# Kernel optimization log

Measured on AMD Instinct MI355X. Metric: run time of the kernel, lower is better.

Reference implementation:

```python
import jax, jax.numpy as jnp
import numpy as np

V, B, N, D, L, H = 30522, 32, 512, 512, 4, 8
HD = D // H
REC = L // 2  # block-recurrent layer index
SCALE = HD ** -0.5


def _ln(x, g, b):
    m = x.mean(-1, keepdims=True)
    v = ((x - m) ** 2).mean(-1, keepdims=True)
    return (x - m) / jnp.sqrt(v + 1e-5) * g + b


def _rope(t):
    # t: [b,h,n,hd]; rotary embedding on token positions (split-half convention)
    n = t.shape[2]
    inv = 1.0 / (10000.0 ** (jnp.arange(0, HD, 2, dtype=jnp.float32) / HD))
    f = jnp.arange(n, dtype=jnp.float32)[:, None] * inv  # [n, hd/2]
    cos, sin = jnp.cos(f), jnp.sin(f)
    t1, t2 = t[..., : HD // 2], t[..., HD // 2 :]
    return jnp.concatenate([t1 * cos - t2 * sin, t2 * cos + t1 * sin], -1)


def _heads(x):
    b, n, _ = x.shape
    return x.reshape(b, n, H, HD).transpose(0, 2, 1, 3)


def _merge(x):
    b, h, n, d = x.shape
    return x.transpose(0, 2, 1, 3).reshape(b, n, h * d)


def _attn(q, k, v, mask):
    s = jnp.einsum('bhid,bhjd->bhij', q, k) * SCALE
    if mask is not None:
        s = jnp.where(mask, s, jnp.float32(-1e9))
    a = jax.nn.softmax(s, axis=-1)
    return jnp.einsum('bhij,bhjd->bhid', a, v)


def setup_inputs() -> dict:
    key = jax.random.key(0)
    ks = jax.random.split(key, 12)
    w = lambda k, shp: jax.random.normal(k, shp, jnp.float32) * 0.02
    return {
        'ids': jax.random.randint(ks[0], (B, N), 0, V),
        'state': jax.random.normal(ks[1], (B, D), jnp.float32),
        'tok_emb': w(ks[2], (V, D)),
        'ln1_g': jnp.ones((L, D), jnp.float32), 'ln1_b': jnp.zeros((L, D), jnp.float32),
        'w_qkv': w(ks[3], (L, D, 3 * D)),
        'w_o': w(ks[4], (L, D, D)),
        'ln2_g': jnp.ones((L, D), jnp.float32), 'ln2_b': jnp.zeros((L, D), jnp.float32),
        'w_ff1': w(ks[5], (L, D, 4 * D)), 'b_ff1': jnp.zeros((L, 4 * D), jnp.float32),
        'w_ff2': w(ks[6], (L, 4 * D, D)), 'b_ff2': jnp.zeros((L, D), jnp.float32),
        's_ln_g': jnp.ones((D,), jnp.float32), 's_ln_b': jnp.zeros((D,), jnp.float32),
        'w_s_qkv': w(ks[7], (D, 3 * D)),
        'w_so': w(ks[8], (D, D)),
        'gate_beta': w(ks[9], (D,)),
        'f_ln_g': jnp.ones((D,), jnp.float32), 'f_ln_b': jnp.zeros((D,), jnp.float32),
        'head_w': w(ks[10], (D, 1)), 'head_b': jnp.zeros((1,), jnp.float32),
    }


def reference(ids, state, tok_emb, ln1_g, ln1_b, w_qkv, w_o, ln2_g, ln2_b,
              w_ff1, b_ff1, w_ff2, b_ff2, s_ln_g, s_ln_b, w_s_qkv, w_so,
              gate_beta, f_ln_g, f_ln_b, head_w, head_b):
    x = tok_emb[ids]                       # [b,n,d]
    s = state[:, None, :]                  # [b,1,d]  (state.unsqueeze(1))
    n = x.shape[1]
    causal = jnp.tril(jnp.ones((n, n), bool))
    for l in range(L):
        h = _ln(x, ln1_g[l], ln1_b[l])
        q, k, v = jnp.split(h @ w_qkv[l], 3, axis=-1)
        q, k, v = _heads(q), _heads(k), _heads(v)
        q, k = _rope(q), _rope(k)
        if l == REC:
            sn = _ln(s, s_ln_g, s_ln_b)
            sq, sk, sv = jnp.split(sn @ w_s_qkv, 3, axis=-1)
            sq, sk, sv = _heads(sq), _heads(sk), _heads(sv)
            # tokens attend over [tokens (causal), state vector (always visible)]
            m = jnp.concatenate([causal, jnp.ones((n, 1), bool)], axis=1)
            out_x = _attn(q, jnp.concatenate([k, sk], 2), jnp.concatenate([v, sv], 2), m)
            x = x + _merge(out_x) @ w_o[l]
            # state attends over [state, all tokens] (no mask)
            out_s = _attn(sq, jnp.concatenate([sk, k], 2), jnp.concatenate([sv, v], 2), None)
            upd = _merge(out_s) @ w_so
            g = jax.nn.sigmoid(gate_beta)   # fixed learned-EMA gate
            s = s * g + upd * (1.0 - g)
        else:
            out_x = _attn(q, k, v, causal)
            x = x + _merge(out_x) @ w_o[l]
        h2 = _ln(x, ln2_g[l], ln2_b[l])
        x = x + jax.nn.gelu(h2 @ w_ff1[l] + b_ff1[l]) @ w_ff2[l] + b_ff2[l]
    x = _ln(x, f_ln_g, f_ln_b)
    state_out = s[:, 0, :]                 # state[0].squeeze()
    logits = x @ head_w + head_b           # [b,n,1]
    out = jax.nn.log_softmax(logits, axis=-1)
    return out, state_out
```

## Files before the change

### kernel.cpp

```cpp
#include <hip/hip_runtime.h>
#include <hip/hip_bf16.h>
#include <math.h>

#define B_ 32
#define N_ 512
#define D_ 512
#define H_ 8
#define HD_ 64
#define QKV_ 1536
#define SCALE_ 0.125f

typedef unsigned short u16;
typedef unsigned int u32;
typedef __attribute__((ext_vector_type(8))) short bf16x8;
typedef __attribute__((ext_vector_type(4))) float f32x4;

#define GLOBAL_AS __attribute__((address_space(1)))
#define LDS_AS __attribute__((address_space(3)))

__device__ __forceinline__ float gelu_f(float x) {
  float u = 0.7978845608028654f * (x + 0.044715f * x * x * x);
  u = fminf(fmaxf(u, -15.f), 15.f);
  float e = __expf(2.f * u);
  float th = 1.f - 2.f * __builtin_amdgcn_rcpf(e + 1.f);
  return 0.5f * x * (1.0f + th);
}

__device__ __forceinline__ u16 f2b(float f) {
  union { float f; u32 u; } v;
  v.f = f;
  u32 r = (v.u + 0x7FFFu + ((v.u >> 16) & 1u)) >> 16;
  return (u16)r;
}

__device__ __forceinline__ float b2f(u16 x) {
  union { u32 u; float f; } v;
  v.u = ((u32)x) << 16;
  return v.f;
}

__device__ __forceinline__ int xcd_swz(int orig, int nwg) {
  int q = nwg >> 3, r = nwg & 7;
  int xcd = orig & 7, idx = orig >> 3;
  return (xcd < r ? xcd * (q + 1) : r * (q + 1) + (xcd - r) * q) + idx;
}

__global__ void k_zero(float* __restrict__ p) {
  p[blockIdx.x * 256 + threadIdx.x] = 0.0f;
}

__global__ void k_rtab(float2* __restrict__ tab) {
  int idx = blockIdx.x * 256 + threadIdx.x;
  int n = idx >> 5, i = idx & 31;
  float inv = powf(10000.0f, -(float)i * (1.0f / 32.0f));
  float f = (float)n * inv;
  float s, c;
  sincosf(f, &s, &c);
  tab[idx] = make_float2(c, s);
}

__global__ void k_embed(const int* __restrict__ ids, const float* __restrict__ emb,
                        float* __restrict__ x) {
  int row = blockIdx.x;
  int id = ids[row];
  const float4* s = (const float4*)(emb + (size_t)id * D_);
  float4* d = (float4*)(x + (size_t)row * D_);
  d[threadIdx.x] = s[threadIdx.x];
}

__global__ void k_wt(const float* __restrict__ W, u16* __restrict__ Wt, int K, int N) {
  __shared__ float tile[32][33];
  int k0 = blockIdx.y * 32, n0 = blockIdx.x * 32;
  int t = threadIdx.x;
  int r = t >> 3, c4 = (t & 7) * 4;
  float4 v = *(const float4*)&W[(size_t)(k0 + r) * N + n0 + c4];
  tile[r][c4] = v.x; tile[r][c4 + 1] = v.y; tile[r][c4 + 2] = v.z; tile[r][c4 + 3] = v.w;
  __syncthreads();
  ushort4 o;
  o.x = f2b(tile[c4 + 0][r]); o.y = f2b(tile[c4 + 1][r]);
  o.z = f2b(tile[c4 + 2][r]); o.w = f2b(tile[c4 + 3][r]);
  *(ushort4*)&Wt[(size_t)(n0 + r) * K + k0 + c4] = o;
}

template <int BF16OUT>
__global__ void k_ln(const float* __restrict__ in, const float* __restrict__ gw,
                     const float* __restrict__ bw, void* __restrict__ outv) {
  int row = blockIdx.x;
  int lane = threadIdx.x;
  const float* p = in + (size_t)row * D_ + lane * 8;
  float4 v0 = *(const float4*)p;
  float4 v1 = *(const float4*)(p + 4);
  float s = v0.x + v0.y + v0.z + v0.w + v1.x + v1.y + v1.z + v1.w;
  float q = v0.x * v0.x + v0.y * v0.y + v0.z * v0.z + v0.w * v0.w +
            v1.x * v1.x + v1.y * v1.y + v1.z * v1.z + v1.w * v1.w;
#pragma unroll
  for (int o = 32; o >= 1; o >>= 1) {
    s += __shfl_xor(s, o);
    q += __shfl_xor(q, o);
  }
  float mean = s * (1.0f / D_);
  float var = q * (1.0f / D_) - mean * mean;
  float rstd = rsqrtf(var + 1e-5f);
  float4 g0 = *(const float4*)(gw + lane * 8);
  float4 g1 = *(const float4*)(gw + lane * 8 + 4);
  float4 b0 = *(const float4*)(bw + lane * 8);
  float4 b1 = *(const float4*)(bw + lane * 8 + 4);
  float o8[8];
  o8[0] = (v0.x - mean) * rstd * g0.x + b0.x;
  o8[1] = (v0.y - mean) * rstd * g0.y + b0.y;
  o8[2] = (v0.z - mean) * rstd * g0.z + b0.z;
  o8[3] = (v0.w - mean) * rstd * g0.w + b0.w;
  o8[4] = (v1.x - mean) * rstd * g1.x + b1.x;
  o8[5] = (v1.y - mean) * rstd * g1.y + b1.y;
  o8[6] = (v1.z - mean) * rstd * g1.z + b1.z;
  o8[7] = (v1.w - mean) * rstd * g1.w + b1.w;
  if (BF16OUT) {
    u16* op = (u16*)outv + (size_t)row * D_ + lane * 8;
    ushort4 a, b;
    a.x = f2b(o8[0]); a.y = f2b(o8[1]); a.z = f2b(o8[2]); a.w = f2b(o8[3]);
    b.x = f2b(o8[4]); b.y = f2b(o8[5]); b.z = f2b(o8[6]); b.w = f2b(o8[7]);
    *(ushort4*)op = a;
    *(ushort4*)(op + 4) = b;
  } else {
    float* op = (float*)outv + (size_t)row * D_ + lane * 8;
    *(float4*)op = make_float4(o8[0], o8[1], o8[2], o8[3]);
    *(float4*)(op + 4) = make_float4(o8[4], o8[5], o8[6], o8[7]);
  }
}

template <int EPI, int BF16OUT>
__global__ __launch_bounds__(256) void k_mgemm(
    const u16* __restrict__ A, const u16* __restrict__ Bt,
    const float* __restrict__ bias, const float* __restrict__ resid,
    void* __restrict__ Cv, int M, int K, int Nc, int nb0) {
  __shared__ u16 As[128 * 32];
  __shared__ u16 Bs[128 * 32];
  int t = threadIdx.x;
  int wave = t >> 6, lane = t & 63;
  int nwg = gridDim.x * gridDim.y;
  int swz = xcd_swz(blockIdx.y * gridDim.x + blockIdx.x, nwg);
  int m0 = (swz / gridDim.x) * 128;
  int n0 = ((swz % gridDim.x) + nb0) * 128;
  int wr = wave >> 1, wc = wave & 1;
  f32x4 acc[4][4] = {};

  int srow = lane >> 2;
  int scol = (lane & 3) * 8;

  for (int k0 = 0; k0 < K; k0 += 32) {
#pragma unroll
    for (int i = 0; i < 2; ++i) {
      int rbase = wave * 32 + i * 16;
      const u16* ga = A + (size_t)(m0 + rbase + srow) * K + k0 + scol;
      __builtin_amdgcn_global_load_lds((const GLOBAL_AS void*)ga,
                                       (LDS_AS void*)&As[rbase * 32], 16, 0, 0);
      const u16* gb = Bt + (size_t)(n0 + rbase + srow) * K + k0 + scol;
      __builtin_amdgcn_global_load_lds((const GLOBAL_AS void*)gb,
                                       (LDS_AS void*)&Bs[rbase * 32], 16, 0, 0);
    }
    __syncthreads();
    bf16x8 af[4], bfr[4];
#pragma unroll
    for (int mi = 0; mi < 4; ++mi)
      af[mi] = *(const bf16x8*)&As[(wr * 64 + mi * 16 + (lane & 15)) * 32 + (lane >> 4) * 8];
#pragma unroll
    for (int ni = 0; ni < 4; ++ni)
      bfr[ni] = *(const bf16x8*)&Bs[(wc * 64 + ni * 16 + (lane & 15)) * 32 + (lane >> 4) * 8];
#pragma unroll
    for (int mi = 0; mi < 4; ++mi)
#pragma unroll
      for (int ni = 0; ni < 4; ++ni)
        acc[mi][ni] = __builtin_amdgcn_mfma_f32_16x16x32_bf16(bfr[ni], af[mi], acc[mi][ni], 0, 0, 0);
    __syncthreads();
  }

#pragma unroll
  for (int mi = 0; mi < 4; ++mi) {
    int m = m0 + wr * 64 + mi * 16 + (lane & 15);
    size_t rowoff = (size_t)m * Nc;
#pragma unroll
    for (int ni = 0; ni < 4; ++ni) {
      int n = n0 + wc * 64 + ni * 16 + (lane >> 4) * 4;
      float v0 = acc[mi][ni][0], v1 = acc[mi][ni][1],
            v2 = acc[mi][ni][2], v3 = acc[mi][ni][3];
      if (EPI == 2 || EPI == 3) {
        float4 bb = *(const float4*)&bias[n];
        v0 += bb.x; v1 += bb.y; v2 += bb.z; v3 += bb.w;
      }
      if (EPI == 2) {
        v0 = gelu_f(v0); v1 = gelu_f(v1); v2 = gelu_f(v2); v3 = gelu_f(v3);
      }
      if (EPI == 1 || EPI == 3) {
        float4 rr = *(const float4*)&resid[rowoff + n];
        v0 += rr.x; v1 += rr.y; v2 += rr.z; v3 += rr.w;
      }
      if (BF16OUT) {
        ushort4 o;
        o.x = f2b(v0); o.y = f2b(v1); o.z = f2b(v2); o.w = f2b(v3);
        *(ushort4*)&((u16*)Cv)[rowoff + n] = o;
      } else {
        *(float4*)&((float*)Cv)[rowoff + n] = make_float4(v0, v1, v2, v3);
      }
    }
  }
}

template <int EPI>
__global__ __launch_bounds__(256) void k_gemm(const float* __restrict__ A,
                                              const float* __restrict__ W,
                                              const float* __restrict__ bias,
                                              const float* __restrict__ resid,
                                              float* __restrict__ C,
                                              int M, int K, int Nc) {
  __shared__ float As[32][68];
  __shared__ float Bs[32][68];
  int t = threadIdx.x;
  int tx = t & 15, ty = t >> 4;
  int m0 = blockIdx.y * 64, n0 = blockIdx.x * 64;
  float acc[4][4] = {};
  int ar = t >> 2, akc = (t & 3) * 8;
  int bkr = t >> 3, bnc = (t & 7) * 8;
  int garow = m0 + ar;
  bool aval = garow < M;
  const float* Aptr = A + (size_t)(aval ? garow : 0) * K + akc;
  const float* Wptr = W + (size_t)bkr * Nc + n0 + bnc;

  for (int k0 = 0; k0 < K; k0 += 32) {
    float4 a0, a1;
    if (aval) {
      a0 = *(const float4*)(Aptr + k0);
      a1 = *(const float4*)(Aptr + k0 + 4);
    } else {
      a0 = make_float4(0.f, 0.f, 0.f, 0.f);
      a1 = a0;
    }
    As[akc + 0][ar] = a0.x; As[akc + 1][ar] = a0.y;
    As[akc + 2][ar] = a0.z; As[akc + 3][ar] = a0.w;
    As[akc + 4][ar] = a1.x; As[akc + 5][ar] = a1.y;
    As[akc + 6][ar] = a1.z; As[akc + 7][ar] = a1.w;
    float4 b0 = *(const float4*)(Wptr + (size_t)k0 * Nc);
    float4 b1 = *(const float4*)(Wptr + (size_t)k0 * Nc + 4);
    *(float4*)&Bs[bkr][bnc] = b0;
    *(float4*)&Bs[bkr][bnc + 4] = b1;
    __syncthreads();
#pragma unroll
    for (int k = 0; k < 32; ++k) {
      float4 av = *(float4*)&As[k][ty * 4];
      float4 bv = *(float4*)&Bs[k][tx * 4];
      float a[4] = {av.x, av.y, av.z, av.w};
      float b[4] = {bv.x, bv.y, bv.z, bv.w};
#pragma unroll
      for (int i = 0; i < 4; ++i)
#pragma unroll
        for (int j = 0; j < 4; ++j) acc[i][j] += a[i] * b[j];
    }
    __syncthreads();
  }
#pragma unroll
  for (int i = 0; i < 4; ++i) {
    int m = m0 + ty * 4 + i;
    if (m >= M) break;
    size_t off = (size_t)m * Nc + n0 + tx * 4;
    float r[4];
#pragma unroll
    for (int j = 0; j < 4; ++j) {
      float v = acc[i][j];
      if (EPI == 2 || EPI == 3) v += bias[n0 + tx * 4 + j];
      if (EPI == 2) v = gelu_f(v);
      if (EPI == 1 || EPI == 3) v += resid[off + j];
      r[j] = v;
    }
    *(float4*)&C[off] = make_float4(r[0], r[1], r[2], r[3]);
  }
}

__global__ __launch_bounds__(512) void k_fattn(const u16* __restrict__ qkv,
                                               const float2* __restrict__ tab,
                                               u16* __restrict__ out) {
  __shared__ u16 Kl[64 * 64];
  __shared__ u16 Vt[64 * 64];
  __shared__ u16 Pl[8][16 * 64];
  int swz = xcd_swz(blockIdx.x, gridDim.x);
  int qt = swz & 3, h = (swz >> 2) & 7, b = swz >> 5;
  int t = threadIdx.x;
  int w = t >> 6, lane = t & 63;
  int c = lane & 15, g = lane >> 4;

  bf16x8 qa[2];
  {
    int n = qt * 128 + w * 16 + c;
    const u16* qptr = qkv + (size_t)(b * N_ + n) * QKV_ + h * HD_ + g * 8;
    union { bf16x8 v; u16 s[8]; } a0, a1, r0, r1;
    a0.v = *(const bf16x8*)qptr;
    a1.v = *(const bf16x8*)(qptr + 32);
    const float2* tb = tab + n * 32 + g * 8;
#pragma unroll
    for (int j = 0; j < 8; ++j) {
      float2 cs = tb[j];
      float lo = b2f(a0.s[j]), hi = b2f(a1.s[j]);
      r0.s[j] = f2b(lo * cs.x - hi * cs.y);
      r1.s[j] = f2b(hi * cs.x + lo * cs.y);
    }
    qa[0] = r0.v;
    qa[1] = r1.v;
  }

  f32x4 O[4] = {};
  float m_r[4], l_r[4];
#pragma unroll
  for (int r = 0; r < 4; ++r) { m_r[r] = -1e30f; l_r[r] = 0.f; }

  int myblk = 2 * qt + (w >> 2);
  int ktmax = 2 * qt + 1;

  for (int kt = 0; kt <= ktmax; ++kt) {
    if (t < 256) {
      int r = t >> 2, i0 = (t & 3) * 8;
      int n = kt * 64 + r;
      const u16* base = qkv + (size_t)(b * N_ + n) * QKV_ + D_ + h * HD_;
      union { bf16x8 v; u16 s[8]; } lo, hi, olo, ohi;
      lo.v = *(const bf16x8*)(base + i0);
      hi.v = *(const bf16x8*)(base + i0 + 32);
      const float2* tb = tab + n * 32 + i0;
#pragma unroll
      for (int j = 0; j < 8; ++j) {
        float2 cs = tb[j];
        float fl = b2f(lo.s[j]), fh = b2f(hi.s[j]);
        olo.s[j] = f2b(fl * cs.x - fh * cs.y);
        ohi.s[j] = f2b(fh * cs.x + fl * cs.y);
      }
      int bb = r * 128 + i0 * 2, sw = (r & 7) << 4;
      *(bf16x8*)((char*)Kl + (bb ^ sw)) = olo.v;
      *(bf16x8*)((char*)Kl + ((bb + 64) ^ sw)) = ohi.v;
    } else {
      int tt = t - 256;
      int kp = (tt >> 3) * 2, d0 = (tt & 7) * 8;
      const u16* v0p = qkv + (size_t)(b * N_ + kt * 64 + kp) * QKV_ + 2 * D_ + h * HD_ + d0;
      const u16* v1p = v0p + QKV_;
      ushort4 x0a = *(const ushort4*)v0p, x0b = *(const ushort4*)(v0p + 4);
      ushort4 x1a = *(const ushort4*)v1p, x1b = *(const ushort4*)(v1p + 4);
      u16 a0[8] = {x0a.x, x0a.y, x0a.z, x0a.w, x0b.x, x0b.y, x0b.z, x0b.w};
      u16 a1[8] = {x1a.x, x1a.y, x1a.z, x1a.w, x1b.x, x1b.y, x1b.z, x1b.w};
      u32* VtW = (u32*)Vt;
#pragma unroll
      for (int j = 0; j < 8; ++j) {
        int d = d0 + j;
        VtW[(d * 32 + (kp >> 1)) ^ ((d & 7) << 2)] = ((u32)a1[j] << 16) | (u32)a0[j];
      }
    }
    __syncthreads();

    if (kt <= myblk) {
      f32x4 s[4] = {};
#pragma unroll
      for (int ks = 0; ks < 2; ++ks) {
#pragma unroll
        for (int nt = 0; nt < 4; ++nt) {
          int krow = nt * 16 + c;
          int byteoff = (krow * 128 + (g * 8 + ks * 32) * 2) ^ ((krow & 7) << 4);
          bf16x8 kb = *(const bf16x8*)((const char*)Kl + byteoff);
          s[nt] = __builtin_amdgcn_mfma_f32_16x16x32_bf16(qa[ks], kb, s[nt], 0, 0, 0);
        }
      }
#pragma unroll
      for (int nt = 0; nt < 4; ++nt)
#pragma unroll
        for (int r = 0; r < 4; ++r) s[nt][r] *= SCALE_;
      if (kt == myblk) {
#pragma unroll
        for (int nt = 0; nt < 4; ++nt)
#pragma unroll
          for (int r = 0; r < 4; ++r)
            if (kt * 64 + nt * 16 + c > qt * 128 + w * 16 + g * 4 + r) s[nt][r] = -1e30f;
      }
      float tm[4], tl[4], fac[4];
#pragma unroll
      for (int r = 0; r < 4; ++r)
        tm[r] = fmaxf(fmaxf(s[0][r], s[1][r]), fmaxf(s[2][r], s[3][r]));
#pragma unroll
      for (int msk = 1; msk <= 8; msk <<= 1)
#pragma unroll
        for (int r = 0; r < 4; ++r)
          tm[r] = fmaxf(tm[r], __shfl_xor(tm[r], msk));
#pragma unroll
      for (int r = 0; r < 4; ++r) {
        float mn = fmaxf(m_r[r], tm[r]);
        fac[r] = __expf(m_r[r] - mn);
        m_r[r] = mn;
        tl[r] = 0.f;
      }
      u16* plw = Pl[w];
#pragma unroll
      for (int nt = 0; nt < 4; ++nt) {
#pragma unroll
        for (int r = 0; r < 4; ++r) {
          float p = __expf(s[nt][r] - m_r[r]);
          tl[r] += p;
          int q = g * 4 + r, kk = nt * 16 + c;
          plw[(q * 64 + kk) ^ ((q & 7) << 3)] = f2b(p);
        }
      }
#pragma unroll
      for (int msk = 1; msk <= 8; msk <<= 1)
#pragma unroll
        for (int r = 0; r < 4; ++r) tl[r] += __shfl_xor(tl[r], msk);
#pragma unroll
      for (int r = 0; r < 4; ++r) l_r[r] = l_r[r] * fac[r] + tl[r];
#pragma unroll
      for (int nt = 0; nt < 4; ++nt)
#pragma unroll
        for (int r = 0; r < 4; ++r) O[nt][r] *= fac[r];

#pragma unroll
      for (int ks = 0; ks < 2; ++ks) {
        int pbyte = (c * 128 + (g * 8 + ks * 32) * 2) ^ ((c & 7) << 4);
        bf16x8 pa = *(const bf16x8*)((const char*)plw + pbyte);
#pragma unroll
        for (int nt = 0; nt < 4; ++nt) {
          int d = nt * 16 + c;
          int vbyte = (d * 128 + (g * 8 + ks * 32) * 2) ^ ((d & 7) << 4);
          bf16x8 vb = *(const bf16x8*)((const char*)Vt + vbyte);
          O[nt] = __builtin_amdgcn_mfma_f32_16x16x32_bf16(pa, vb, O[nt], 0, 0, 0);
        }
      }
    }
    __syncthreads();
  }

  u16* dst = out + (size_t)(b * N_ + qt * 128 + w * 16) * D_ + h * HD_;
#pragma unroll
  for (int nt = 0; nt < 4; ++nt) {
#pragma unroll
    for (int r = 0; r < 4; ++r) {
      int q = g * 4 + r;
      dst[(size_t)q * D_ + nt * 16 + c] = f2b(O[nt][r] / l_r[r]);
    }
  }
}

__global__ __launch_bounds__(128) void k_state_attn(const float* __restrict__ sqkv,
                                                    const u16* __restrict__ qkv,
                                                    const float2* __restrict__ tab,
                                                    float* __restrict__ outs) {
  int h = blockIdx.x, b = blockIdx.y;
  __shared__ float sq[HD_];
  __shared__ float sc[513];
  __shared__ float red[128];
  int t = threadIdx.x;
  if (t < HD_) sq[t] = sqkv[(size_t)b * QKV_ + h * HD_ + t];
  __syncthreads();
  for (int j = t; j < 513; j += 128) {
    float acc = 0.f;
    if (j == 0) {
      const float* kp = sqkv + (size_t)b * QKV_ + D_ + h * HD_;
#pragma unroll
      for (int d = 0; d < HD_; ++d) acc += sq[d] * kp[d];
    } else {
      const u16* kp = qkv + (size_t)(b * N_ + j - 1) * QKV_ + D_ + h * HD_;
      const float2* tb = tab + (size_t)(j - 1) * 32;
#pragma unroll
      for (int d = 0; d < 32; ++d) {
        float2 cs = tb[d];
        float klo = b2f(kp[d]), khi = b2f(kp[d + 32]);
        acc += sq[d] * (klo * cs.x - khi * cs.y) + sq[d + 32] * (khi * cs.x + klo * cs.y);
      }
    }
    sc[j] = acc * SCALE_;
  }
  __syncthreads();
  float m = -1e30f;
  for (int j = t; j < 513; j += 128) m = fmaxf(m, sc[j]);
  red[t] = m;
  __syncthreads();
  for (int s = 64; s > 0; s >>= 1) {
    if (t < s) red[t] = fmaxf(red[t], red[t + s]);
    __syncthreads();
  }
  m = red[0];
  __syncthreads();
  float sum = 0.f;
  for (int j = t; j < 513; j += 128) {
    float p = expf(sc[j] - m);
    sc[j] = p;
    sum += p;
  }
  red[t] = sum;
  __syncthreads();
  for (int s = 64; s > 0; s >>= 1) {
    if (t < s) red[t] += red[t + s];
    __syncthreads();
  }
  float tot = red[0];
  if (t < HD_) {
    int d = t;
    float acc = sc[0] * sqkv[(size_t)b * QKV_ + 2 * D_ + h * HD_ + d];
    for (int j = 1; j <= N_; ++j)
      acc += sc[j] * b2f(qkv[(size_t)(b * N_ + j - 1) * QKV_ + 2 * D_ + h * HD_ + d]);
    outs[(size_t)b * D_ + h * HD_ + d] = acc / tot;
  }
}

__global__ void k_gate(const float* __restrict__ state, const float* __restrict__ upd,
                       const float* __restrict__ beta, float* __restrict__ out2) {
  int idx = blockIdx.x * 256 + threadIdx.x;
  int c = idx & (D_ - 1);
  float g = __builtin_amdgcn_rcpf(1.0f + __expf(-beta[c]));
  out2[idx] = state[idx] * g + upd[idx] * (1.0f - g);
}

extern "C" void kernel_launch(void* const* d_in, const int* in_sizes, int n_in,
                              void* d_out, int out_size, void* d_ws, size_t ws_size,
                              hipStream_t stream) {
  (void)in_sizes; (void)n_in; (void)out_size; (void)ws_size;
  const int* ids = (const int*)d_in[0];
  const float* state = (const float*)d_in[1];
  const float* tok_emb = (const float*)d_in[2];
  const float* ln1_g = (const float*)d_in[3];
  const float* ln1_b = (const float*)d_in[4];
  const float* w_qkv = (const float*)d_in[5];
  const float* w_o = (const float*)d_in[6];
  const float* ln2_g = (const float*)d_in[7];
  const float* ln2_b = (const float*)d_in[8];
  const float* w_ff1 = (const float*)d_in[9];
  const float* b_ff1 = (const float*)d_in[10];
  const float* w_ff2 = (const float*)d_in[11];
  const float* b_ff2 = (const float*)d_in[12];
  const float* s_ln_g = (const float*)d_in[13];
  const float* s_ln_b = (const float*)d_in[14];
  const float* w_s_qkv = (const float*)d_in[15];
  const float* w_so = (const float*)d_in[16];
  const float* gate_beta = (const float*)d_in[17];

  float* out0 = (float*)d_out;
  float* out1 = (float*)d_out + 16384;

  float* ws = (float*)d_ws;
  float* x = ws;
  u16* qkv_bf = (u16*)(ws + 8388608);
  u16* mid_bf = qkv_bf;
  u16* h_bf = (u16*)(ws + 25165824);
  u16* ao_bf = (u16*)(ws + 29360128);
  u16* wq_t = (u16*)(ws + 33554432);
  u16* wo_t = (u16*)(ws + 34734080);
  u16* wf1_t = (u16*)(ws + 34996224);
  u16* wf2_t = (u16*)(ws + 36044800);
  float* sln = ws + 37093376;
  float* sqkv = sln + 16384;
  float* souts = sqkv + 49152;
  float* supd = souts + 16384;
  float2* tab = (float2*)(ws + 37191680);

  const int M = B_ * N_;

  k_zero<<<dim3(64), dim3(256), 0, stream>>>(out0);
  k_rtab<<<dim3(64), dim3(256), 0, stream>>>(tab);

  for (int l = 0; l < 3; ++l)
    k_wt<<<dim3(48, 16), dim3(256), 0, stream>>>(w_qkv + (size_t)l * D_ * QKV_,
                                                 wq_t + (size_t)l * QKV_ * D_, D_, QKV_);
  for (int l = 0; l < 2; ++l) {
    k_wt<<<dim3(16, 16), dim3(256), 0, stream>>>(w_o + (size_t)l * D_ * D_,
                                                 wo_t + (size_t)l * D_ * D_, D_, D_);
    k_wt<<<dim3(64, 16), dim3(256), 0, stream>>>(w_ff1 + (size_t)l * D_ * 4 * D_,
                                                 wf1_t + (size_t)l * 4 * D_ * D_, D_, 4 * D_);
    k_wt<<<dim3(16, 64), dim3(256), 0, stream>>>(w_ff2 + (size_t)l * 4 * D_ * D_,
                                                 wf2_t + (size_t)l * D_ * 4 * D_, 4 * D_, D_);
  }

  k_embed<<<dim3(M), dim3(128), 0, stream>>>(ids, tok_emb, x);

  for (int l = 0; l < 3; ++l) {
    k_ln<1><<<dim3(M), dim3(64), 0, stream>>>(x, ln1_g + l * D_, ln1_b + l * D_, h_bf);
    if (l == 2) {
      k_mgemm<0, 1><<<dim3(8, 128), dim3(256), 0, stream>>>(
          h_bf, wq_t + (size_t)l * QKV_ * D_, nullptr, nullptr, qkv_bf, M, D_, QKV_, 4);
      break;
    }
    k_mgemm<0, 1><<<dim3(12, 128), dim3(256), 0, stream>>>(
        h_bf, wq_t + (size_t)l * QKV_ * D_, nullptr, nullptr, qkv_bf, M, D_, QKV_, 0);
    k_fattn<<<dim3((N_ / 128) * H_ * B_), dim3(512), 0, stream>>>(qkv_bf, tab, ao_bf);
    k_mgemm<1, 0><<<dim3(4, 128), dim3(256), 0, stream>>>(
        ao_bf, wo_t + (size_t)l * D_ * D_, nullptr, x, x, M, D_, D_, 0);
    k_ln<1><<<dim3(M), dim3(64), 0, stream>>>(x, ln2_g + l * D_, ln2_b + l * D_, h_bf);
    k_mgemm<2, 1><<<dim3(16, 128), dim3(256), 0, stream>>>(
        h_bf, wf1_t + (size_t)l * 4 * D_ * D_, b_ff1 + l * 4 * D_, nullptr, mid_bf, M, D_, 4 * D_, 0);
    k_mgemm<3, 0><<<dim3(4, 128), dim3(256), 0, stream>>>(
        mid_bf, wf2_t + (size_t)l * D_ * 4 * D_, b_ff2 + l * D_, x, x, M, 4 * D_, D_, 0);
  }

  k_ln<0><<<dim3(B_), dim3(64), 0, stream>>>(state, s_ln_g, s_ln_b, sln);
  k_gemm<0><<<dim3(24, 1), dim3(256), 0, stream>>>(
      sln, w_s_qkv, nullptr, nullptr, sqkv, B_, D_, QKV_);
  k_state_attn<<<dim3(H_, B_), dim3(128), 0, stream>>>(sqkv, qkv_bf, tab, souts);
  k_gemm<0><<<dim3(8, 1), dim3(256), 0, stream>>>(
      souts, w_so, nullptr, nullptr, supd, B_, D_, D_);
  k_gate<<<dim3(64), dim3(256), 0, stream>>>(state, supd, gate_beta, out1);
}
```

Before: 743.2 us.

## Double-buffer GEMM LDS tiles, merge prep kernels, pack four LN rows per block

The bf16 MFMA GEMM now keeps two LDS buffers and issues the next K-slice's global-to-LDS loads before computing the current one, dropping one barrier per iteration so load latency can overlap with compute. The zero-fill, RoPE table and all weight transposes are merged into one launch to cut kernel launch overhead. LayerNorm now handles four rows per 256-thread block instead of one row per 64-thread block. The double buffer doubles GEMM LDS use, which may lower occupancy.

Result: faster. 670.0 us (-9.8%).

```diff
diff --git a/kernel.cpp b/kernel.cpp
--- a/kernel.cpp
+++ b/kernel.cpp
@@ -45,33 +45,49 @@
   return (xcd < r ? xcd * (q + 1) : r * (q + 1) + (xcd - r) * q) + idx;
 }
 
-__global__ void k_zero(float* __restrict__ p) {
-  p[blockIdx.x * 256 + threadIdx.x] = 0.0f;
-}
-
-__global__ void k_rtab(float2* __restrict__ tab) {
-  int idx = blockIdx.x * 256 + threadIdx.x;
-  int n = idx >> 5, i = idx & 31;
-  float inv = powf(10000.0f, -(float)i * (1.0f / 32.0f));
-  float f = (float)n * inv;
-  float s, c;
-  sincosf(f, &s, &c);
-  tab[idx] = make_float2(c, s);
-}
-
-__global__ void k_embed(const int* __restrict__ ids, const float* __restrict__ emb,
-                        float* __restrict__ x) {
-  int row = blockIdx.x;
-  int id = ids[row];
-  const float4* s = (const float4*)(emb + (size_t)id * D_);
-  float4* d = (float4*)(x + (size_t)row * D_);
-  d[threadIdx.x] = s[threadIdx.x];
-}
-
-__global__ void k_wt(const float* __restrict__ W, u16* __restrict__ Wt, int K, int N) {
+__global__ void k_prep(const float* __restrict__ w_qkv, const float* __restrict__ w_o,
+                       const float* __restrict__ w_ff1, const float* __restrict__ w_ff2,
+                       u16* __restrict__ wq_t, u16* __restrict__ wo_t,
+                       u16* __restrict__ wf1_t, u16* __restrict__ wf2_t,
+                       float* __restrict__ out0, float2* __restrict__ tab) {
   __shared__ float tile[32][33];
-  int k0 = blockIdx.y * 32, n0 = blockIdx.x * 32;
+  int bid = blockIdx.x;
   int t = threadIdx.x;
+  if (bid < 64) {
+    int idx = bid * 256 + t;
+    out0[idx] = 0.f;
+    int n = idx >> 5, i = idx & 31;
+    float inv = powf(10000.0f, -(float)i * (1.0f / 32.0f));
+    float f = (float)n * inv;
+    float s, c;
+    sincosf(f, &s, &c);
+    tab[idx] = make_float2(c, s);
+    return;
+  }
+  int b2 = bid - 64;
+  const float* W;
+  u16* Wt;
+  int K, N;
+  if (b2 < 2304) {
+    int l = b2 / 768; b2 -= l * 768;
+    W = w_qkv + (size_t)l * D_ * QKV_; Wt = wq_t + (size_t)l * QKV_ * D_;
+    K = D_; N = QKV_;
+  } else if (b2 < 2816) {
+    b2 -= 2304; int l = b2 >> 8; b2 &= 255;
+    W = w_o + (size_t)l * D_ * D_; Wt = wo_t + (size_t)l * D_ * D_;
+    K = D_; N = D_;
+  } else if (b2 < 4864) {
+    b2 -= 2816; int l = b2 >> 10; b2 &= 1023;
+    W = w_ff1 + (size_t)l * D_ * 4 * D_; Wt = wf1_t + (size_t)l * 4 * D_ * D_;
+    K = D_; N = 4 * D_;
+  } else {
+    b2 -= 4864; int l = b2 >> 10; b2 &= 1023;
+    W = w_ff2 + (size_t)l * 4 * D_ * D_; Wt = wf2_t + (size_t)l * D_ * 4 * D_;
+    K = 4 * D_; N = D_;
+  }
+  int nbx = N >> 5;
+  int bx = b2 % nbx, by = b2 / nbx;
+  int k0 = by * 32, n0 = bx * 32;
   int r = t >> 3, c4 = (t & 7) * 4;
   float4 v = *(const float4*)&W[(size_t)(k0 + r) * N + n0 + c4];
   tile[r][c4] = v.x; tile[r][c4 + 1] = v.y; tile[r][c4 + 2] = v.z; tile[r][c4 + 3] = v.w;
@@ -82,11 +98,20 @@
   *(ushort4*)&Wt[(size_t)(n0 + r) * K + k0 + c4] = o;
 }
 
+__global__ void k_embed(const int* __restrict__ ids, const float* __restrict__ emb,
+                        float* __restrict__ x) {
+  int row = blockIdx.x;
+  int id = ids[row];
+  const float4* s = (const float4*)(emb + (size_t)id * D_);
+  float4* d = (float4*)(x + (size_t)row * D_);
+  d[threadIdx.x] = s[threadIdx.x];
+}
+
 template <int BF16OUT>
 __global__ void k_ln(const float* __restrict__ in, const float* __restrict__ gw,
                      const float* __restrict__ bw, void* __restrict__ outv) {
-  int row = blockIdx.x;
-  int lane = threadIdx.x;
+  int row = blockIdx.x * 4 + (threadIdx.x >> 6);
+  int lane = threadIdx.x & 63;
   const float* p = in + (size_t)row * D_ + lane * 8;
   float4 v0 = *(const float4*)p;
   float4 v1 = *(const float4*)(p + 4);
@@ -133,8 +158,8 @@
     const u16* __restrict__ A, const u16* __restrict__ Bt,
     const float* __restrict__ bias, const float* __restrict__ resid,
     void* __restrict__ Cv, int M, int K, int Nc, int nb0) {
-  __shared__ u16 As[128 * 32];
-  __shared__ u16 Bs[128 * 32];
+  __shared__ u16 As[2][128 * 32];
+  __shared__ u16 Bs[2][128 * 32];
   int t = threadIdx.x;
   int wave = t >> 6, lane = t & 63;
   int nwg = gridDim.x * gridDim.y;
@@ -146,26 +171,37 @@
 
   int srow = lane >> 2;
   int scol = (lane & 3) * 8;
-
-  for (int k0 = 0; k0 < K; k0 += 32) {
-#pragma unroll
-    for (int i = 0; i < 2; ++i) {
-      int rbase = wave * 32 + i * 16;
-      const u16* ga = A + (size_t)(m0 + rbase + srow) * K + k0 + scol;
-      __builtin_amdgcn_global_load_lds((const GLOBAL_AS void*)ga,
-                                       (LDS_AS void*)&As[rbase * 32], 16, 0, 0);
-      const u16* gb = Bt + (size_t)(n0 + rbase + srow) * K + k0 + scol;
-      __builtin_amdgcn_global_load_lds((const GLOBAL_AS void*)gb,
-                                       (LDS_AS void*)&Bs[rbase * 32], 16, 0, 0);
-    }
-    __syncthreads();
+  const u16* gaBase = A + (size_t)(m0 + wave * 32 + srow) * K + scol;
+  const u16* gbBase = Bt + (size_t)(n0 + wave * 32 + srow) * K + scol;
+
+#define STAGE_MG(bsel, kk)                                                     \
+  {                                                                            \
+    _Pragma("unroll") for (int i_ = 0; i_ < 2; ++i_) {                         \
+      int rbase_ = wave * 32 + i_ * 16;                                        \
+      __builtin_amdgcn_global_load_lds(                                        \
+          (const GLOBAL_AS void*)(gaBase + (size_t)(i_ * 16) * K + (kk)),      \
+          (LDS_AS void*)&As[bsel][rbase_ * 32], 16, 0, 0);                     \
+      __builtin_amdgcn_global_load_lds(                                        \
+          (const GLOBAL_AS void*)(gbBase + (size_t)(i_ * 16) * K + (kk)),      \
+          (LDS_AS void*)&Bs[bsel][rbase_ * 32], 16, 0, 0);                     \
+    }                                                                          \
+  }
+
+  int nIter = K >> 5;
+  STAGE_MG(0, 0);
+  __syncthreads();
+  for (int it = 0; it < nIter; ++it) {
+    int cur = it & 1;
+    if (it + 1 < nIter) STAGE_MG(cur ^ 1, (it + 1) << 5);
+    const u16* as = As[cur];
+    const u16* bs = Bs[cur];
     bf16x8 af[4], bfr[4];
 #pragma unroll
     for (int mi = 0; mi < 4; ++mi)
-      af[mi] = *(const bf16x8*)&As[(wr * 64 + mi * 16 + (lane & 15)) * 32 + (lane >> 4) * 8];
+      af[mi] = *(const bf16x8*)&as[(wr * 64 + mi * 16 + (lane & 15)) * 32 + (lane >> 4) * 8];
 #pragma unroll
     for (int ni = 0; ni < 4; ++ni)
-      bfr[ni] = *(const bf16x8*)&Bs[(wc * 64 + ni * 16 + (lane & 15)) * 32 + (lane >> 4) * 8];
+      bfr[ni] = *(const bf16x8*)&bs[(wc * 64 + ni * 16 + (lane & 15)) * 32 + (lane >> 4) * 8];
 #pragma unroll
     for (int mi = 0; mi < 4; ++mi)
 #pragma unroll
@@ -173,6 +209,7 @@
         acc[mi][ni] = __builtin_amdgcn_mfma_f32_16x16x32_bf16(bfr[ni], af[mi], acc[mi][ni], 0, 0, 0);
     __syncthreads();
   }
+#undef STAGE_MG
 
 #pragma unroll
   for (int mi = 0; mi < 4; ++mi) {
@@ -552,25 +589,12 @@
 
   const int M = B_ * N_;
 
-  k_zero<<<dim3(64), dim3(256), 0, stream>>>(out0);
-  k_rtab<<<dim3(64), dim3(256), 0, stream>>>(tab);
-
-  for (int l = 0; l < 3; ++l)
-    k_wt<<<dim3(48, 16), dim3(256), 0, stream>>>(w_qkv + (size_t)l * D_ * QKV_,
-                                                 wq_t + (size_t)l * QKV_ * D_, D_, QKV_);
-  for (int l = 0; l < 2; ++l) {
-    k_wt<<<dim3(16, 16), dim3(256), 0, stream>>>(w_o + (size_t)l * D_ * D_,
-                                                 wo_t + (size_t)l * D_ * D_, D_, D_);
-    k_wt<<<dim3(64, 16), dim3(256), 0, stream>>>(w_ff1 + (size_t)l * D_ * 4 * D_,
-                                                 wf1_t + (size_t)l * 4 * D_ * D_, D_, 4 * D_);
-    k_wt<<<dim3(16, 64), dim3(256), 0, stream>>>(w_ff2 + (size_t)l * 4 * D_ * D_,
-                                                 wf2_t + (size_t)l * D_ * 4 * D_, 4 * D_, D_);
-  }
-
+  k_prep<<<dim3(6976), dim3(256), 0, stream>>>(w_qkv, w_o, w_ff1, w_ff2,
+                                               wq_t, wo_t, wf1_t, wf2_t, out0, tab);
   k_embed<<<dim3(M), dim3(128), 0, stream>>>(ids, tok_emb, x);
 
   for (int l = 0; l < 3; ++l) {
-    k_ln<1><<<dim3(M), dim3(64), 0, stream>>>(x, ln1_g + l * D_, ln1_b + l * D_, h_bf);
+    k_ln<1><<<dim3(M / 4), dim3(256), 0, stream>>>(x, ln1_g + l * D_, ln1_b + l * D_, h_bf);
     if (l == 2) {
       k_mgemm<0, 1><<<dim3(8, 128), dim3(256), 0, stream>>>(
           h_bf, wq_t + (size_t)l * QKV_ * D_, nullptr, nullptr, qkv_bf, M, D_, QKV_, 4);
@@ -581,14 +605,14 @@
     k_fattn<<<dim3((N_ / 128) * H_ * B_), dim3(512), 0, stream>>>(qkv_bf, tab, ao_bf);
     k_mgemm<1, 0><<<dim3(4, 128), dim3(256), 0, stream>>>(
         ao_bf, wo_t + (size_t)l * D_ * D_, nullptr, x, x, M, D_, D_, 0);
-    k_ln<1><<<dim3(M), dim3(64), 0, stream>>>(x, ln2_g + l * D_, ln2_b + l * D_, h_bf);
+    k_ln<1><<<dim3(M / 4), dim3(256), 0, stream>>>(x, ln2_g + l * D_, ln2_b + l * D_, h_bf);
     k_mgemm<2, 1><<<dim3(16, 128), dim3(256), 0, stream>>>(
         h_bf, wf1_t + (size_t)l * 4 * D_ * D_, b_ff1 + l * 4 * D_, nullptr, mid_bf, M, D_, 4 * D_, 0);
     k_mgemm<3, 0><<<dim3(4, 128), dim3(256), 0, stream>>>(
         mid_bf, wf2_t + (size_t)l * D_ * 4 * D_, b_ff2 + l * D_, x, x, M, 4 * D_, D_, 0);
   }
 
-  k_ln<0><<<dim3(B_), dim3(64), 0, stream>>>(state, s_ln_g, s_ln_b, sln);
+  k_ln<0><<<dim3(B_ / 4), dim3(256), 0, stream>>>(state, s_ln_g, s_ln_b, sln);
   k_gemm<0><<<dim3(24, 1), dim3(256), 0, stream>>>(
       sln, w_s_qkv, nullptr, nullptr, sqkv, B_, D_, QKV_);
   k_state_attn<<<dim3(H_, B_), dim3(128), 0, stream>>>(sqkv, qkv_bf, tab, souts);
```
